# Performance work log

Measured on AMD Instinct MI355X. Metric: run time of the kernel, lower is better.

The kernel has to match this reference:

```python
import jax, jax.numpy as jnp
import numpy as np

B, DIM, HEADS, H, W = 4, 64, 8, 512, 512


def _conv(x, w, groups=1):
    # NCHW x, OIHW w, stride 1, SAME padding (padding=k//2 in torch)
    return jax.lax.conv_general_dilated(
        x, w, (1, 1), 'SAME', feature_group_count=groups,
        dimension_numbers=('NCHW', 'OIHW', 'NCHW'))


def _dwt_haar(x):
    # single-level orthonormal haar on even-sized NCHW input
    a = x[..., 0::2, 0::2]; b = x[..., 0::2, 1::2]
    c = x[..., 1::2, 0::2]; d = x[..., 1::2, 1::2]
    LL = (a + b + c + d) * 0.5
    LH = (-a - b + c + d) * 0.5
    HL = (-a + b - c + d) * 0.5
    HH = (a - b - c + d) * 0.5
    return LL, LH, HL, HH


def _idwt_haar(LL, LH, HL, HH):
    a = (LL - LH - HL + HH) * 0.5
    b = (LL - LH + HL - HH) * 0.5
    c = (LL + LH - HL - HH) * 0.5
    d = (LL + LH + HL + HH) * 0.5
    Bn, C, h, w = LL.shape
    even = jnp.stack([a, b], -1).reshape(Bn, C, h, 2 * w)  # rows 0::2
    odd = jnp.stack([c, d], -1).reshape(Bn, C, h, 2 * w)   # rows 1::2
    return jnp.stack([even, odd], -2).reshape(Bn, C, 2 * h, 2 * w)


def _l2norm(x, eps=1e-12):
    n = jnp.sqrt(jnp.sum(x * x, axis=-1, keepdims=True))
    return x / jnp.maximum(n, eps)


def setup_inputs() -> dict:
    key = jax.random.key(0)
    ks = jax.random.split(key, 8)
    def w(k, shape):
        fan_in = shape[1] * shape[2] * shape[3]
        return jax.random.normal(k, shape, jnp.float32) * (1.0 / np.sqrt(fan_in))
    return {
        'x': jax.random.normal(ks[0], (B, DIM, H, W), jnp.float32),
        'w_hc1': w(ks[1], (2 * DIM, DIM, 3, 3)),        # groups=2 over 2*dim channels
        'w_hc2': w(ks[2], (DIM, 2 * DIM, 1, 1)),
        'w_ho': w(ks[3], (3 * DIM, DIM, 3, 3)),          # groups=3 over 3*dim channels
        'w_qkv': w(ks[4], (3 * DIM, DIM, 1, 1)),
        'w_dw': w(ks[5], (3 * DIM, 1, 3, 3)),            # depthwise, groups=3*dim
        'w_proj': w(ks[6], (DIM, DIM, 1, 1)),
        'temperature': jnp.ones((HEADS, 1, 1), jnp.float32),
    }


def reference(x, w_hc1, w_hc2, w_ho, w_qkv, w_dw, w_proj, temperature):
    LL, LH, HL, HH = _dwt_haar(x)

    # high-frequency (LH,HL) filter branch
    hv = jnp.concatenate([LH, HL], axis=1)
    filter_hv = jax.nn.relu(_conv(jax.nn.relu(_conv(hv, w_hc1, groups=2)), w_hc2))

    # qkv from LL: 1x1 conv then depthwise 3x3
    qkv = _conv(_conv(LL, w_qkv), w_dw, groups=3 * DIM)
    q, k, v = jnp.split(qkv, 3, axis=1)
    b, c, h, w = q.shape
    v = v * filter_hv + v

    ch = c // HEADS
    q = q.reshape(b, HEADS, ch, h * w)
    k = k.reshape(b, HEADS, ch, h * w)
    v = v.reshape(b, HEADS, ch, h * w)
    q = _l2norm(q)
    k = _l2norm(k)

    attn = jnp.einsum('bhcn,bhdn->bhcd', q, k) * temperature  # [b,heads,ch,ch]
    attn = jax.nn.softmax(attn, axis=-1)
    out = jnp.einsum('bhcd,bhdn->bhcn', attn, v).reshape(b, c, h, w)
    out = _conv(out, w_proj)

    # high-frequency output branch
    yh = jax.nn.relu(_conv(jnp.concatenate([LH, HL, HH], axis=1), w_ho, groups=3))
    LH2, HL2, HH2 = jnp.split(yh, 3, axis=1)

    return _idwt_haar(out, LH2, HL2, HH2)
```

## Files before the change

### kernel.cpp

```cpp
#include <hip/hip_runtime.h>
#include <hip/hip_bf16.h>

#define BN 4
#define DIM 64
#define NHEADS 8
#define HH 256
#define WH 256
#define NP (HH*WH)
#define HF 512
#define WF 512

#define PD 258
#define PROW (PD*64)
#define PPLANE ((size_t)PD*PD*64)

typedef __attribute__((ext_vector_type(8))) short bfx8;
typedef __attribute__((ext_vector_type(8))) unsigned short u16x8;
typedef __attribute__((ext_vector_type(4))) unsigned short u16x4;
typedef __attribute__((ext_vector_type(4))) float f32x4;

static __device__ __forceinline__ short f2bf(float f) {
    unsigned u = __float_as_uint(f);
    unsigned r = (u + 0x7FFFu + ((u >> 16) & 1u)) >> 16;
    return (short)r;
}
static __device__ __forceinline__ float bfu(unsigned short u) {
    return __uint_as_float((unsigned)u << 16);
}

__global__ __launch_bounds__(256) void k_setup(unsigned short* __restrict__ tiled16,
                                               const float* __restrict__ w_ho,
                                               const float* __restrict__ w_hc1,
                                               const float* __restrict__ w_hc2,
                                               const float* __restrict__ w_qkv,
                                               short* __restrict__ wrHO,
                                               short* __restrict__ wrHC1,
                                               short* __restrict__ wrHC2,
                                               short* __restrict__ wrQKV) {
    int bx = blockIdx.x, tid = threadIdx.x;
    if (bx < 16) {
        char* base = (char*)(tiled16 + (size_t)bx * PPLANE);
        const int ROWB = PROW * 2;
        for (int k = tid; k < 8224; k += 256) {
            char* dst;
            if (k < 2064) dst = base + (size_t)k * 16;
            else if (k < 4128) dst = base + (size_t)257 * ROWB + (size_t)(k - 2064) * 16;
            else if (k < 6176) { int r = (k - 4128) >> 3, s = (k - 4128) & 7;
                dst = base + (size_t)(r + 1) * ROWB + (size_t)s * 16; }
            else { int r = (k - 6176) >> 3, s = (k - 6176) & 7;
                dst = base + (size_t)(r + 1) * ROWB + 257 * 128 + (size_t)s * 16; }
            *(uint4*)dst = (uint4){0, 0, 0, 0};
        }
        return;
    }
    if (bx < 16 + 432 + 288) {
        const float* w = (bx < 448) ? w_ho : w_hc1;
        short* wrep = (bx < 448) ? wrHO : wrHC1;
        int t = (bx - ((bx < 448) ? 16 : 448)) * 256 + tid;
        unsigned g   = (unsigned)t / 36864u;
        unsigned r1  = (unsigned)t % 36864u;
        unsigned tap = r1 / 4096u;
        unsigned r2  = r1 % 4096u;
        unsigned icb = r2 / 512u;
        unsigned r3  = r2 % 512u;
        unsigned oc  = r3 >> 3;
        unsigned j   = r3 & 7u;
        wrep[t] = f2bf(w[(((size_t)g * 64 + oc) * 64 + icb * 8u + j) * 9 + tap]);
        return;
    }
    if (bx < 16 + 432 + 288 + 32) {
        int t = (bx - 736) * 256 + tid;
        int j = t & 7, gr = t >> 3, o16 = gr & 15, X = gr >> 4;
        int icb = X % 16, oct = X / 16;
        wrHC2[t] = f2bf(w_hc2[(size_t)(oct * 16 + o16) * 128 + icb * 8 + j]);
        return;
    }
    {
        int t = (bx - 768) * 256 + tid;
        int j = t & 7, gr = t >> 3, o16 = gr & 15, X = gr >> 4;
        int icb = X % 8, oct = X / 8;
        wrQKV[t] = f2bf(w_qkv[(size_t)(oct * 16 + o16) * 64 + icb * 8 + j]);
    }
}

__global__ __launch_bounds__(256) void k_dwt(const float* __restrict__ x,
                                             unsigned short* __restrict__ tiled,
                                             unsigned short* __restrict__ llp) {
    __shared__ unsigned short lds[3 * 128 * 64] __attribute__((aligned(16)));
    const int tid = threadIdx.x;
    const int pid = blockIdx.x;
    const int b = blockIdx.y;
    const int y0 = (pid >> 4) * 8, x0 = (pid & 15) * 16;
    const int quad = tid & 127;
    const int qy = quad >> 4, qx = quad & 15;
    const int gy = y0 + qy, gx = x0 + qx;
    const int ich = tid >> 7;
    unsigned short* llb = llp + (size_t)b * PPLANE + ((size_t)(gy + 1) * PD + (gx + 1)) * 64;

#pragma unroll 4
    for (int it = 0; it < 16; ++it) {
        int ic = it * 4 + ich * 2;
        unsigned g = (((unsigned)(ic >> 3)) + (unsigned)gx + 2u * (unsigned)gy) & 7u;
        unsigned swz = (unsigned)quad * 64 + (g << 3) + (unsigned)(ic & 7);
        unsigned pk[3], pll;
#pragma unroll
        for (int s = 0; s < 2; ++s) {
            const float* px = x + (((size_t)(b * 64 + ic + s) * HF) + 2 * gy) * WF + 2 * gx;
            float2 e0 = *(const float2*)px;
            float2 e1 = *(const float2*)(px + WF);
            float a = e0.x, bb = e0.y, c = e1.x, d = e1.y;
            unsigned ll = (unsigned short)f2bf(( a + bb + c + d) * 0.5f);
            unsigned lh = (unsigned short)f2bf((-a - bb + c + d) * 0.5f);
            unsigned hl = (unsigned short)f2bf((-a + bb - c + d) * 0.5f);
            unsigned hh = (unsigned short)f2bf(( a - bb - c + d) * 0.5f);
            if (s == 0) { pll = ll; pk[0] = lh; pk[1] = hl; pk[2] = hh; }
            else { pll |= ll << 16; pk[0] |= lh << 16; pk[1] |= hl << 16; pk[2] |= hh << 16; }
        }
        *(unsigned*)&lds[swz]          = pk[0];
        *(unsigned*)&lds[8192 + swz]   = pk[1];
        *(unsigned*)&lds[16384 + swz]  = pk[2];
        *(unsigned*)&llb[(g << 3) + (unsigned)(ic & 7)] = pll;
    }
    __syncthreads();
#pragma unroll
    for (int it = 0; it < 12; ++it) {
        int cch = tid + it * 256;
        int p = cch >> 10, rem = cch & 1023;
        int row = rem >> 7, col = rem & 127;
        unsigned short* dst = tiled + ((size_t)(b * 3 + p) * PD + (y0 + row + 1)) * PROW
                                    + (size_t)(x0 + 1) * 64 + (size_t)col * 8;
        *(uint4*)dst = *(const uint4*)((const char*)lds + (size_t)cch * 16);
    }
}

template <int LAYOUT>
__global__ __launch_bounds__(256) void k_gconv3x3_mfma(const unsigned short* __restrict__ tiled,
                                                       const bfx8* __restrict__ wr,
                                                       unsigned short* __restrict__ out, int OC) {
    __shared__ short lds_in[324 * 64] __attribute__((aligned(16)));
    const int tid = threadIdx.x;
    const int l = tid & 63, wv = tid >> 6;
    const int tile = blockIdx.x;
    const int x0 = (tile & 15) * 16, y0 = (tile >> 4) * 16;
    const int g = blockIdx.y, b = blockIdx.z;
    const unsigned short* src = tiled + (size_t)(b * 3 + g) * PPLANE;

#pragma unroll
    for (int it = 0; it < 10; ++it) {
        int cch = it * 256 + tid;
        unsigned row = (unsigned)cch / 144u, col = (unsigned)cch % 144u;
        const unsigned short* ga = src + (size_t)(y0 + row) * PROW + (size_t)x0 * 64 + (size_t)col * 8;
        __builtin_amdgcn_global_load_lds(
            (const __attribute__((address_space(1))) void*)ga,
            (__attribute__((address_space(3))) void*)((char*)lds_in + (size_t)(it * 256 + wv * 64) * 16),
            16, 0, 0);
    }
    if (tid < 32) {
        int cch = 2560 + tid;
        unsigned row = (unsigned)cch / 144u, col = (unsigned)cch % 144u;
        const unsigned short* ga = src + (size_t)(y0 + row) * PROW + (size_t)x0 * 64 + (size_t)col * 8;
        *(uint4*)((char*)lds_in + (size_t)cch * 16) = *(const uint4*)ga;
    }
    __syncthreads();

    f32x4 acc[4][4];
#pragma unroll
    for (int i = 0; i < 4; ++i)
#pragma unroll
        for (int j = 0; j < 4; ++j) acc[i][j] = (f32x4){0.f, 0.f, 0.f, 0.f};

    const int lx = l & 15, lq = l >> 4;
#pragma unroll
    for (int c = 0; c < 2; ++c) {
        const int icb = c * 4 + lq;
#pragma unroll
        for (int tap = 0; tap < 9; ++tap) {
            const int dy = tap / 3, dx = tap % 3;
            const size_t wbase = ((size_t)(g * 9 + tap) * 8 + icb) * 64 + lx;
            bfx8 b0 = wr[wbase];
            bfx8 b1 = wr[wbase + 16];
            bfx8 b2 = wr[wbase + 32];
            bfx8 b3 = wr[wbase + 48];
#pragma unroll
            for (int pg = 0; pg < 4; ++pg) {
                int hy = wv * 4 + pg + dy, hx = lx + dx;
                int hp = hy * 18 + hx;
                const bfx8* ap = (const bfx8*)&lds_in[hp * 64 + (((icb + hx + 2 * hy + 5) & 7) << 3)];
                bfx8 a = *ap;
                acc[pg][0] = __builtin_amdgcn_mfma_f32_16x16x32_bf16(a, b0, acc[pg][0], 0, 0, 0);
                acc[pg][1] = __builtin_amdgcn_mfma_f32_16x16x32_bf16(a, b1, acc[pg][1], 0, 0, 0);
                acc[pg][2] = __builtin_amdgcn_mfma_f32_16x16x32_bf16(a, b2, acc[pg][2], 0, 0, 0);
                acc[pg][3] = __builtin_amdgcn_mfma_f32_16x16x32_bf16(a, b3, acc[pg][3], 0, 0, 0);
            }
        }
    }

#pragma unroll
    for (int pg = 0; pg < 4; ++pg) {
#pragma unroll
        for (int ocg = 0; ocg < 4; ++ocg) {
            f32x4 v = acc[pg][ocg];
            if (LAYOUT == 0) {
                unsigned short* op = out + ((size_t)(b * 256 + tile) * OC + g * 64 + ocg * 16 + lx) * 256
                                         + (wv * 4 + pg) * 16 + lq * 4;
                ushort4 s4;
                s4.x = (unsigned short)f2bf(fmaxf(v.x, 0.f));
                s4.y = (unsigned short)f2bf(fmaxf(v.y, 0.f));
                s4.z = (unsigned short)f2bf(fmaxf(v.z, 0.f));
                s4.w = (unsigned short)f2bf(fmaxf(v.w, 0.f));
                *(ushort4*)op = s4;
            } else {
                int icT = g * 64 + ocg * 16 + lx;
                int g16 = icT >> 3;
                unsigned short* tb = out + ((size_t)(b * 256 + tile) * 256) * 128;
                int innerb = (wv * 4 + pg) * 16 + lq * 4;
                float vr[4] = {v.x, v.y, v.z, v.w};
#pragma unroll
                for (int r = 0; r < 4; ++r) {
                    int inn = innerb + r;
                    tb[(size_t)inn * 128 + (((g16 + inn) & 15) << 3) + (icT & 7)] =
                        (unsigned short)f2bf(fmaxf(vr[r], 0.f));
                }
            }
        }
    }
}

template <int CIN, int OC, bool RELU>
__global__ __launch_bounds__(256) void k_conv1x1_mfma(const unsigned short* __restrict__ inT,
                                                      const bfx8* __restrict__ wr,
                                                      unsigned short* __restrict__ out) {
    constexpr int KB = CIN / 8;
    constexpr int KC = CIN / 32;
    constexpr int NOCT = OC / 16;
    __shared__ short ldsA[256 * CIN] __attribute__((aligned(16)));
    const int tid = threadIdx.x;
    const int l = tid & 63, wv = tid >> 6;
    const int tile = blockIdx.x, b = blockIdx.y;
    const unsigned short* src = inT + ((size_t)(b * 256 + tile) * 256) * CIN;
    constexpr int ITER = (256 * CIN / 8) / 256;
#pragma unroll
    for (int it = 0; it < ITER; ++it) {
        int cc = it * 256 + tid;
        __builtin_amdgcn_global_load_lds(
            (const __attribute__((address_space(1))) void*)(src + (size_t)cc * 8),
            (__attribute__((address_space(3))) void*)((char*)ldsA + (size_t)(it * 256 + wv * 64) * 16),
            16, 0, 0);
    }
    __syncthreads();

    const int lx = l & 15, lq = l >> 4;
    const int x0 = (tile & 15) * 16, y0 = (tile >> 4) * 16;
#pragma unroll
    for (int o4 = 0; o4 < NOCT / 4; ++o4) {
        f32x4 acc[4][4];
#pragma unroll
        for (int i = 0; i < 4; ++i)
#pragma unroll
            for (int j = 0; j < 4; ++j) acc[i][j] = (f32x4){0.f, 0.f, 0.f, 0.f};
#pragma unroll
        for (int c = 0; c < KC; ++c) {
            const int icb = c * 4 + lq;
            bfx8 bf[4];
#pragma unroll
            for (int ot = 0; ot < 4; ++ot)
                bf[ot] = wr[(size_t)(((o4 * 4 + ot) * KB + icb) * 16) + lx];
#pragma unroll
            for (int pg = 0; pg < 4; ++pg) {
                int inner = (wv * 4 + pg) * 16 + lx;
                const bfx8* ap = (const bfx8*)&ldsA[inner * CIN + (((icb + inner) & (KB - 1)) << 3)];
                bfx8 a = *ap;
                acc[pg][0] = __builtin_amdgcn_mfma_f32_16x16x32_bf16(a, bf[0], acc[pg][0], 0, 0, 0);
                acc[pg][1] = __builtin_amdgcn_mfma_f32_16x16x32_bf16(a, bf[1], acc[pg][1], 0, 0, 0);
                acc[pg][2] = __builtin_amdgcn_mfma_f32_16x16x32_bf16(a, bf[2], acc[pg][2], 0, 0, 0);
                acc[pg][3] = __builtin_amdgcn_mfma_f32_16x16x32_bf16(a, bf[3], acc[pg][3], 0, 0, 0);
            }
        }
#pragma unroll
        for (int pg = 0; pg < 4; ++pg)
#pragma unroll
            for (int ot = 0; ot < 4; ++ot) {
                int oc = (o4 * 4 + ot) * 16 + lx;
                unsigned short* op = out + ((size_t)b * OC + oc) * NP
                                         + (size_t)(y0 + wv * 4 + pg) * WH + x0 + lq * 4;
                f32x4 v = acc[pg][ot];
                ushort4 s4;
                s4.x = (unsigned short)f2bf(RELU ? fmaxf(v.x, 0.f) : v.x);
                s4.y = (unsigned short)f2bf(RELU ? fmaxf(v.y, 0.f) : v.y);
                s4.z = (unsigned short)f2bf(RELU ? fmaxf(v.z, 0.f) : v.z);
                s4.w = (unsigned short)f2bf(RELU ? fmaxf(v.w, 0.f) : v.w);
                *(ushort4*)op = s4;
            }
    }
}

__global__ __launch_bounds__(256) void k_qkv_fused(const unsigned short* __restrict__ llp,
                                                   const bfx8* __restrict__ wrq,
                                                   const float* __restrict__ wdw,
                                                   const unsigned short* __restrict__ filt,
                                                   unsigned short* __restrict__ qkv) {
    __shared__ short ldsA[336 * 64] __attribute__((aligned(16)));
    __shared__ float ldsW[192 * 9];
    const int tid = threadIdx.x;
    const int l = tid & 63, wv = tid >> 6;
    const int tile = blockIdx.x, b = blockIdx.y;
    const int x0 = (tile & 15) * 16, y0 = (tile >> 4) * 16;
    const unsigned short* src = llp + (size_t)b * PPLANE;

#pragma unroll
    for (int it = 0; it < 10; ++it) {
        int cch = it * 256 + tid;
        unsigned row = (unsigned)cch / 144u, col = (unsigned)cch % 144u;
        const unsigned short* ga = src + (size_t)(y0 + row) * PROW + (size_t)x0 * 64 + (size_t)col * 8;
        __builtin_amdgcn_global_load_lds(
            (const __attribute__((address_space(1))) void*)ga,
            (__attribute__((address_space(3))) void*)((char*)ldsA + (size_t)(it * 256 + wv * 64) * 16),
            16, 0, 0);
    }
    if (tid < 32) {
        int cch = 2560 + tid;
        unsigned row = (unsigned)cch / 144u, col = (unsigned)cch % 144u;
        const unsigned short* ga = src + (size_t)(y0 + row) * PROW + (size_t)x0 * 64 + (size_t)col * 8;
        *(uint4*)((char*)ldsA + (size_t)cch * 16) = *(const uint4*)ga;
    }
    for (int k = tid; k < 1728; k += 256) ldsW[k] = wdw[k];
    __syncthreads();

    const int lx = l & 15, lq = l >> 4;
    bfx8 af[6][2];
#pragma unroll
    for (int m = 0; m < 6; ++m) {
        int mt = wv + 4 * m;
        if (mt < 21) {
            int hp = mt * 16 + lx;
            int hy = hp / 18, hx = hp - hy * 18;
#pragma unroll
            for (int kc = 0; kc < 2; ++kc) {
                int icb = kc * 4 + lq;
                af[m][kc] = *(const bfx8*)&ldsA[hp * 64 + (((icb + hx + 2 * hy + 5) & 7) << 3)];
            }
        }
    }
    __syncthreads();

    for (int g3 = 0; g3 < 3; ++g3) {
        bfx8 bw[2][4];
#pragma unroll
        for (int kc = 0; kc < 2; ++kc)
#pragma unroll
            for (int nt = 0; nt < 4; ++nt)
                bw[kc][nt] = wrq[(size_t)(((g3 * 4 + nt) * 8) + kc * 4 + lq) * 16 + lx];
#pragma unroll
        for (int m = 0; m < 6; ++m) {
            int mt = wv + 4 * m;
            if (mt < 21) {
                f32x4 acc[4];
#pragma unroll
                for (int nt = 0; nt < 4; ++nt) acc[nt] = (f32x4){0.f, 0.f, 0.f, 0.f};
#pragma unroll
                for (int kc = 0; kc < 2; ++kc) {
                    bfx8 a = af[m][kc];
#pragma unroll
                    for (int nt = 0; nt < 4; ++nt)
                        acc[nt] = __builtin_amdgcn_mfma_f32_16x16x32_bf16(a, bw[kc][nt], acc[nt], 0, 0, 0);
                }
#pragma unroll
                for (int nt = 0; nt < 4; ++nt) {
                    int ocl = nt * 16 + lx;
                    float vr[4] = {acc[nt].x, acc[nt].y, acc[nt].z, acc[nt].w};
#pragma unroll
                    for (int r = 0; r < 4; ++r) {
                        int hp2 = mt * 16 + lq * 4 + r;
                        int hy2 = hp2 / 18, hx2 = hp2 - hy2 * 18;
                        ldsA[hp2 * 64 + ((((ocl >> 3) + hx2 + 2 * hy2) & 7) << 3) + (ocl & 7)] =
                            f2bf(vr[r]);
                    }
                }
            }
        }
        __syncthreads();
        {
            const int ch = l, chg = g3 * 64 + ch;
            float w9[9];
#pragma unroll
            for (int t = 0; t < 9; ++t) w9[t] = ldsW[chg * 9 + t];
#pragma unroll
            for (int yy = 0; yy < 4; ++yy) {
                int y = wv * 4 + yy;
                float ln[3][18];
#pragma unroll
                for (int hr = 0; hr < 3; ++hr) {
                    int hy = y + hr;
#pragma unroll
                    for (int hx = 0; hx < 18; ++hx)
                        ln[hr][hx] = bfu((unsigned short)ldsA[(hy * 18 + hx) * 64 +
                                         ((((ch >> 3) + hx + 2 * hy) & 7) << 3) + (ch & 7)]);
                }
                float ox[16];
#pragma unroll
                for (int xx = 0; xx < 16; ++xx) {
                    float s = 0.f;
#pragma unroll
                    for (int hr = 0; hr < 3; ++hr)
#pragma unroll
                        for (int dx = 0; dx < 3; ++dx)
                            s = fmaf(ln[hr][xx + dx], w9[hr * 3 + dx], s);
                    ox[xx] = s;
                }
                if (g3 == 2) {
                    const unsigned short* fp = filt + ((size_t)b * 64 + ch) * NP
                                                    + (size_t)(y0 + y) * WH + x0;
                    u16x8 f0 = *(const u16x8*)fp;
                    u16x8 f1 = *(const u16x8*)(fp + 8);
#pragma unroll
                    for (int k = 0; k < 8; ++k) ox[k]     = fmaf(ox[k],     bfu(f0[k]), ox[k]);
#pragma unroll
                    for (int k = 0; k < 8; ++k) ox[8 + k] = fmaf(ox[8 + k], bfu(f1[k]), ox[8 + k]);
                }
                u16x8 s0, s1;
#pragma unroll
                for (int k = 0; k < 8; ++k) { s0[k] = (unsigned short)f2bf(ox[k]);
                                              s1[k] = (unsigned short)f2bf(ox[8 + k]); }
                unsigned short* op = qkv + ((size_t)b * 192 + chg) * NP + (size_t)(y0 + y) * WH + x0;
                *(u16x8*)op = s0;
                *(u16x8*)(op + 8) = s1;
            }
        }
        __syncthreads();
    }
}

__global__ __launch_bounds__(256) void k_attn_dot(const unsigned short* __restrict__ qkv,
                                                  float* __restrict__ praw,
                                                  float* __restrict__ praw2) {
    int bhd = blockIdx.x, sp = blockIdx.y;
    int b = bhd >> 3, hd = bhd & 7;
    const unsigned short* qb = qkv + ((size_t)b * 192 + hd * 8) * NP;
    const unsigned short* kb = qkv + ((size_t)b * 192 + 64 + hd * 8) * NP;
    float acc[64], acc2[16];
#pragma unroll
    for (int i = 0; i < 64; ++i) acc[i] = 0.f;
#pragma unroll
    for (int i = 0; i < 16; ++i) acc2[i] = 0.f;
    int n0 = sp * (NP / 8);
#pragma unroll 2
    for (int it = 0; it < 4; ++it) {
        int n = n0 + (it * 256 + threadIdx.x) * 8;
        u16x8 q8[8], k8[8];
#pragma unroll
        for (int c2 = 0; c2 < 8; ++c2) q8[c2] = *(const u16x8*)(qb + (size_t)c2 * NP + n);
#pragma unroll
        for (int d2 = 0; d2 < 8; ++d2) k8[d2] = *(const u16x8*)(kb + (size_t)d2 * NP + n);
#pragma unroll
        for (int j = 0; j < 8; ++j) {
            float qv[8], kv[8];
#pragma unroll
            for (int c2 = 0; c2 < 8; ++c2) qv[c2] = bfu(q8[c2][j]);
#pragma unroll
            for (int d2 = 0; d2 < 8; ++d2) kv[d2] = bfu(k8[d2][j]);
#pragma unroll
            for (int c2 = 0; c2 < 8; ++c2) {
                acc2[c2] = fmaf(qv[c2], qv[c2], acc2[c2]);
#pragma unroll
                for (int d2 = 0; d2 < 8; ++d2)
                    acc[c2 * 8 + d2] = fmaf(qv[c2], kv[d2], acc[c2 * 8 + d2]);
            }
#pragma unroll
            for (int d2 = 0; d2 < 8; ++d2) acc2[8 + d2] = fmaf(kv[d2], kv[d2], acc2[8 + d2]);
        }
    }
    __shared__ float red[4][64];
#pragma unroll
    for (int i = 0; i < 64; ++i) {
        float v = acc[i];
#pragma unroll
        for (int off = 32; off; off >>= 1) v += __shfl_down(v, off);
        if ((threadIdx.x & 63) == 0) red[threadIdx.x >> 6][i] = v;
    }
    __syncthreads();
    if (threadIdx.x < 64)
        praw[((size_t)sp * 32 + bhd) * 64 + threadIdx.x] =
            red[0][threadIdx.x] + red[1][threadIdx.x] + red[2][threadIdx.x] + red[3][threadIdx.x];
    __syncthreads();
#pragma unroll
    for (int i = 0; i < 16; ++i) {
        float v = acc2[i];
#pragma unroll
        for (int off = 32; off; off >>= 1) v += __shfl_down(v, off);
        if ((threadIdx.x & 63) == 0) red[threadIdx.x >> 6][i] = v;
    }
    __syncthreads();
    if (threadIdx.x < 16)
        praw2[((size_t)sp * 32 + bhd) * 16 + threadIdx.x] =
            red[0][threadIdx.x] + red[1][threadIdx.x] + red[2][threadIdx.x] + red[3][threadIdx.x];
}

__global__ __launch_bounds__(64) void k_attn_soft(const float* __restrict__ praw,
                                                  const float* __restrict__ praw2,
                                                  const float* __restrict__ temp,
                                                  float* __restrict__ attn) {
    int bhd = blockIdx.x;
    int hd = bhd & 7;
    int t = threadIdx.x, c = t >> 3, d = t & 7;
    float s = 0.f, sq = 0.f, sk = 0.f;
    for (int sp = 0; sp < 8; ++sp) {
        s  += praw[((size_t)sp * 32 + bhd) * 64 + t];
        sq += praw2[((size_t)sp * 32 + bhd) * 16 + c];
        sk += praw2[((size_t)sp * 32 + bhd) * 16 + 8 + d];
    }
    float nq = fmaxf(sqrtf(sq), 1e-12f);
    float nk = fmaxf(sqrtf(sk), 1e-12f);
    s = s / (nq * nk) * temp[hd];
    __shared__ float sm[64];
    __shared__ float se[64];
    sm[t] = s;
    __syncthreads();
    float mx = -1e30f;
#pragma unroll
    for (int dd = 0; dd < 8; ++dd) mx = fmaxf(mx, sm[c * 8 + dd]);
    float e = __expf(s - mx);
    se[t] = e;
    __syncthreads();
    float sum = 0.f;
#pragma unroll
    for (int dd = 0; dd < 8; ++dd) sum += se[c * 8 + dd];
    attn[(size_t)bhd * 64 + t] = e / sum;
}

__global__ __launch_bounds__(256) void k_prep_attn(const float* __restrict__ attn,
                                                   const float* __restrict__ wproj,
                                                   short* __restrict__ mrep) {
    int b = blockIdx.x, t = threadIdx.x;
    const float* ab = attn + (size_t)b * 512;
#pragma unroll
    for (int i = 0; i < 16; ++i) {
        int idx = t * 16 + i;
        int j = idx & 7, o16 = (idx >> 3) & 15, icb = (idx >> 7) & 7, oct = idx >> 10;
        int oc = oct * 16 + o16;
        float m = 0.f;
#pragma unroll
        for (int c8 = 0; c8 < 8; ++c8)
            m = fmaf(wproj[(size_t)oc * 64 + icb * 8 + c8], ab[icb * 64 + c8 * 8 + j], m);
        mrep[(size_t)b * 4096 + idx] = f2bf(m);
    }
}

__global__ __launch_bounds__(256) void k_attnout_idwt(const unsigned short* __restrict__ qkv,
                                                      const bfx8* __restrict__ mrep,
                                                      const unsigned short* __restrict__ yht,
                                                      float* __restrict__ out) {
    const int tid = threadIdx.x;
    const int l = tid & 63, wv = tid >> 6;
    const int lx = l & 15, lq = l >> 4;
    const int tile = blockIdx.x, b = blockIdx.y;
    const int x0 = (tile & 15) * 16, y0 = (tile >> 4) * 16;
    const unsigned short* vb = qkv + ((size_t)b * 192 + 128) * NP;
    const bfx8* mb = mrep + (size_t)b * 512;

    bfx8 bw[2][4];
#pragma unroll
    for (int kc = 0; kc < 2; ++kc)
#pragma unroll
        for (int nt = 0; nt < 4; ++nt)
            bw[kc][nt] = mb[(nt * 8 + kc * 4 + lq) * 16 + lx];

    const unsigned short* yb = yht + (size_t)(b * 256 + tile) * 192 * 256;

#pragma unroll
    for (int pg = 0; pg < 4; ++pg) {
        const int mt = wv * 4 + pg;
        const int y = y0 + mt;
        const unsigned short* vrow = vb + (size_t)y * WH + x0 + lx;
        bfx8 a0, a1;
#pragma unroll
        for (int j = 0; j < 8; ++j) a0[j] = (short)vrow[(size_t)(lq * 8 + j) * NP];
#pragma unroll
        for (int j = 0; j < 8; ++j) a1[j] = (short)vrow[(size_t)(32 + lq * 8 + j) * NP];

        f32x4 acc[4];
#pragma unroll
        for (int nt = 0; nt < 4; ++nt) acc[nt] = (f32x4){0.f, 0.f, 0.f, 0.f};
#pragma unroll
        for (int nt = 0; nt < 4; ++nt) {
            acc[nt] = __builtin_amdgcn_mfma_f32_16x16x32_bf16(a0, bw[0][nt], acc[nt], 0, 0, 0);
            acc[nt] = __builtin_amdgcn_mfma_f32_16x16x32_bf16(a1, bw[1][nt], acc[nt], 0, 0, 0);
        }
#pragma unroll
        for (int nt = 0; nt < 4; ++nt) {
            const int oc = nt * 16 + lx;
            const int inner = mt * 16 + lq * 4;
            const unsigned short* yp = yb + (size_t)oc * 256 + inner;
            u16x4 lh4 = *(const u16x4*)yp;
            u16x4 hl4 = *(const u16x4*)(yp + (size_t)64 * 256);
            u16x4 hh4 = *(const u16x4*)(yp + (size_t)128 * 256);
            float e0[8], e1[8];
#pragma unroll
            for (int r = 0; r < 4; ++r) {
                float s  = acc[nt][r];
                float LH = bfu(lh4[r]), HL = bfu(hl4[r]), HHv = bfu(hh4[r]);
                e0[2 * r]     = (s - LH - HL + HHv) * 0.5f;
                e0[2 * r + 1] = (s - LH + HL - HHv) * 0.5f;
                e1[2 * r]     = (s + LH - HL - HHv) * 0.5f;
                e1[2 * r + 1] = (s + LH + HL + HHv) * 0.5f;
            }
            float* o0 = out + ((size_t)(b * 64 + oc) * HF + 2 * y) * WF + 2 * (x0 + lq * 4);
            *(float4*)o0            = *(float4*)&e0[0];
            *(float4*)(o0 + 4)      = *(float4*)&e0[4];
            *(float4*)(o0 + WF)     = *(float4*)&e1[0];
            *(float4*)(o0 + WF + 4) = *(float4*)&e1[4];
        }
    }
}

extern "C" void kernel_launch(void* const* d_in, const int* in_sizes, int n_in,
                              void* d_out, int out_size, void* d_ws, size_t ws_size,
                              hipStream_t stream) {
    const float* x      = (const float*)d_in[0];
    const float* w_hc1  = (const float*)d_in[1];
    const float* w_hc2  = (const float*)d_in[2];
    const float* w_ho   = (const float*)d_in[3];
    const float* w_qkv  = (const float*)d_in[4];
    const float* w_dw   = (const float*)d_in[5];
    const float* w_proj = (const float*)d_in[6];
    const float* temp   = (const float*)d_in[7];
    float* out = (float*)d_out;

    char* base = (char*)d_ws;
    unsigned short* TILED = (unsigned short*)(base + 0);
    unsigned short* LLP   = (unsigned short*)(base + 102242304ULL);
    unsigned short* YH    = (unsigned short*)(base + 136323072ULL);
    unsigned short* T1T   = (unsigned short*)(base + 236986368ULL);
    unsigned short* FILT  = (unsigned short*)(base + 304095232ULL);
    unsigned short* QKV   = (unsigned short*)(base + 337649664ULL);
    float*          PRAW  = (float*)(base + 438312960ULL);
    float*          PRAW2 = (float*)(base + 438378496ULL);
    float*          ATTN  = (float*)(base + 438394880ULL);
    short* WREP_HO  = (short*)(base + 438403072ULL);
    short* WREP_HC1 = (short*)(base + 438624256ULL);
    short* WREP_HC2 = (short*)(base + 438771712ULL);
    short* WREP_QKV = (short*)(base + 438788096ULL);
    short* MREP     = (short*)(base + 438812672ULL);

    k_setup<<<816, 256, 0, stream>>>(TILED, w_ho, w_hc1, w_hc2, w_qkv,
                                     WREP_HO, WREP_HC1, WREP_HC2, WREP_QKV);
    k_dwt<<<dim3(512, BN), 256, 0, stream>>>(x, TILED, LLP);
    k_gconv3x3_mfma<0><<<dim3(256, 3, BN), 256, 0, stream>>>(TILED, (const bfx8*)WREP_HO, YH, 192);
    k_gconv3x3_mfma<1><<<dim3(256, 2, BN), 256, 0, stream>>>(TILED, (const bfx8*)WREP_HC1, T1T, 128);
    k_conv1x1_mfma<128, 64, true><<<dim3(256, BN), 256, 0, stream>>>(T1T, (const bfx8*)WREP_HC2, FILT);
    k_qkv_fused<<<dim3(256, BN), 256, 0, stream>>>(LLP, (const bfx8*)WREP_QKV, w_dw, FILT, QKV);
    k_attn_dot<<<dim3(32, 8), 256, 0, stream>>>(QKV, PRAW, PRAW2);
    k_attn_soft<<<32, 64, 0, stream>>>(PRAW, PRAW2, temp, ATTN);
    k_prep_attn<<<BN, 256, 0, stream>>>(ATTN, w_proj, MREP);
    k_attnout_idwt<<<dim3(256, BN), 256, 0, stream>>>(QKV, (const bfx8*)MREP, YH, out);
}
```

Baseline: 602.9 us.

## Fuse q·kᵀ Gram and norm partials into qkv kernel, drop q/k writeback

```diff
diff --git a/kernel.cpp b/kernel.cpp
--- a/kernel.cpp
+++ b/kernel.cpp
@@ -298,9 +298,12 @@
                                                    const bfx8* __restrict__ wrq,
                                                    const float* __restrict__ wdw,
                                                    const unsigned short* __restrict__ filt,
-                                                   unsigned short* __restrict__ qkv) {
+                                                   unsigned short* __restrict__ vt,
+                                                   float* __restrict__ praw,
+                                                   float* __restrict__ praw2) {
     __shared__ short ldsA[336 * 64] __attribute__((aligned(16)));
-    __shared__ float ldsW[192 * 9];
+    __shared__ short qsave[64 * 256] __attribute__((aligned(16)));
+    __shared__ float ssq[2][4][64];
     const int tid = threadIdx.x;
     const int l = tid & 63, wv = tid >> 6;
     const int tile = blockIdx.x, b = blockIdx.y;
@@ -323,7 +326,6 @@
         const unsigned short* ga = src + (size_t)(y0 + row) * PROW + (size_t)x0 * 64 + (size_t)col * 8;
         *(uint4*)((char*)ldsA + (size_t)cch * 16) = *(const uint4*)ga;
     }
-    for (int k = tid; k < 1728; k += 256) ldsW[k] = wdw[k];
     __syncthreads();
 
     const int lx = l & 15, lq = l >> 4;
@@ -379,120 +381,120 @@
             }
         }
         __syncthreads();
-        {
-            const int ch = l, chg = g3 * 64 + ch;
-            float w9[9];
-#pragma unroll
-            for (int t = 0; t < 9; ++t) w9[t] = ldsW[chg * 9 + t];
+        const int ch = l, chg = g3 * 64 + ch;
+        float w9[9];
+#pragma unroll
+        for (int t = 0; t < 9; ++t) w9[t] = wdw[chg * 9 + t];
+        float s2 = 0.f;
+        u16x8 kpk[4][2];
+#pragma unroll
+        for (int yy = 0; yy < 4; ++yy) {
+            int y = wv * 4 + yy;
+            float ln[3][18];
+#pragma unroll
+            for (int hr = 0; hr < 3; ++hr) {
+                int hy = y + hr;
+#pragma unroll
+                for (int hx = 0; hx < 18; ++hx)
+                    ln[hr][hx] = bfu((unsigned short)ldsA[(hy * 18 + hx) * 64 +
+                                     ((((ch >> 3) + hx + 2 * hy) & 7) << 3) + (ch & 7)]);
+            }
+            float ox[16];
+#pragma unroll
+            for (int xx = 0; xx < 16; ++xx) {
+                float s = 0.f;
+#pragma unroll
+                for (int hr = 0; hr < 3; ++hr)
+#pragma unroll
+                    for (int dx = 0; dx < 3; ++dx)
+                        s = fmaf(ln[hr][xx + dx], w9[hr * 3 + dx], s);
+                ox[xx] = s;
+            }
+            if (g3 == 2) {
+                const unsigned short* fp = filt + ((size_t)b * 64 + ch) * NP
+                                                + (size_t)(y0 + y) * WH + x0;
+                u16x8 f0 = *(const u16x8*)fp;
+                u16x8 f1 = *(const u16x8*)(fp + 8);
+#pragma unroll
+                for (int k = 0; k < 8; ++k) ox[k]     = fmaf(ox[k],     bfu(f0[k]), ox[k]);
+#pragma unroll
+                for (int k = 0; k < 8; ++k) ox[8 + k] = fmaf(ox[8 + k], bfu(f1[k]), ox[8 + k]);
+                unsigned short* vb = vt + ((size_t)(b * 256 + tile) * 256 + (size_t)y * 16) * 64 + ch;
+#pragma unroll
+                for (int xx = 0; xx < 16; ++xx) vb[xx * 64] = (unsigned short)f2bf(ox[xx]);
+            } else {
+#pragma unroll
+                for (int xx = 0; xx < 16; ++xx) s2 = fmaf(ox[xx], ox[xx], s2);
+                if (g3 == 0) {
+#pragma unroll
+                    for (int xx = 0; xx < 16; ++xx) {
+                        int px = y * 16 + xx;
+                        qsave[ch * 256 + ((((px >> 3) + ch) & 31) << 3) + (px & 7)] =
+                            f2bf(ox[xx]);
+                    }
+                } else {
+#pragma unroll
+                    for (int xx = 0; xx < 8; ++xx)  kpk[yy][0][xx] = (unsigned short)f2bf(ox[xx]);
+#pragma unroll
+                    for (int xx = 0; xx < 8; ++xx)  kpk[yy][1][xx] = (unsigned short)f2bf(ox[8 + xx]);
+                }
+            }
+        }
+        if (g3 == 0) ssq[0][wv][ch] = s2;
+        if (g3 == 1) {
+            ssq[1][wv][ch] = s2;
+            __syncthreads();
+            short* kbuf = ldsA;
 #pragma unroll
             for (int yy = 0; yy < 4; ++yy) {
                 int y = wv * 4 + yy;
-                float ln[3][18];
-#pragma unroll
-                for (int hr = 0; hr < 3; ++hr) {
-                    int hy = y + hr;
-#pragma unroll
-                    for (int hx = 0; hx < 18; ++hx)
-                        ln[hr][hx] = bfu((unsigned short)ldsA[(hy * 18 + hx) * 64 +
-                                         ((((ch >> 3) + hx + 2 * hy) & 7) << 3) + (ch & 7)]);
+#pragma unroll
+                for (int xx = 0; xx < 16; ++xx) {
+                    int px = y * 16 + xx;
+                    kbuf[ch * 256 + ((((px >> 3) + ch) & 31) << 3) + (px & 7)] =
+                        (short)kpk[yy][xx >> 3][xx & 7];
                 }
-                float ox[16];
-#pragma unroll
-                for (int xx = 0; xx < 16; ++xx) {
-                    float s = 0.f;
-#pragma unroll
-                    for (int hr = 0; hr < 3; ++hr)
-#pragma unroll
-                        for (int dx = 0; dx < 3; ++dx)
-                            s = fmaf(ln[hr][xx + dx], w9[hr * 3 + dx], s);
-                    ox[xx] = s;
+            }
+            __syncthreads();
+            f32x4 sacc[4];
+#pragma unroll
+            for (int t16 = 0; t16 < 4; ++t16) sacc[t16] = (f32x4){0.f, 0.f, 0.f, 0.f};
+#pragma unroll
+            for (int kc2 = 0; kc2 < 2; ++kc2) {
+                int kc = wv * 2 + kc2;
+#pragma unroll
+                for (int t16 = 0; t16 < 4; ++t16) {
+                    int chh = t16 * 16 + lx;
+                    int go = chh * 256 + (((kc * 4 + lq + chh) & 31) << 3);
+                    bfx8 aq = *(const bfx8*)&qsave[go];
+                    bfx8 bk = *(const bfx8*)&kbuf[go];
+                    sacc[t16] = __builtin_amdgcn_mfma_f32_16x16x32_bf16(aq, bk, sacc[t16], 0, 0, 0);
                 }
-                if (g3 == 2) {
-                    const unsigned short* fp = filt + ((size_t)b * 64 + ch) * NP
-                                                    + (size_t)(y0 + y) * WH + x0;
-                    u16x8 f0 = *(const u16x8*)fp;
-                    u16x8 f1 = *(const u16x8*)(fp + 8);
-#pragma unroll
-                    for (int k = 0; k < 8; ++k) ox[k]     = fmaf(ox[k],     bfu(f0[k]), ox[k]);
-#pragma unroll
-                    for (int k = 0; k < 8; ++k) ox[8 + k] = fmaf(ox[8 + k], bfu(f1[k]), ox[8 + k]);
+            }
+            __syncthreads();
+            float* sred = (float*)qsave;
+#pragma unroll
+            for (int t16 = 0; t16 < 4; ++t16)
+                *(f32x4*)&sred[((wv * 4 + t16) * 64 + l) * 4] = sacc[t16];
+            __syncthreads();
+            {
+                int t16r = tid >> 6, lr = tid & 63;
+                f32x4 s0 = *(const f32x4*)&sred[((0 * 4 + t16r) * 64 + lr) * 4];
+                f32x4 s1 = *(const f32x4*)&sred[((1 * 4 + t16r) * 64 + lr) * 4];
+                f32x4 s2r = *(const f32x4*)&sred[((2 * 4 + t16r) * 64 + lr) * 4];
+                f32x4 s3 = *(const f32x4*)&sred[((3 * 4 + t16r) * 64 + lr) * 4];
+                f32x4 sum = s0 + s1 + s2r + s3;
+                *(f32x4*)&praw[(((size_t)(b * 256 + tile) * 4 + t16r) * 64 + lr) * 4] = sum;
+                if (tid < 128) {
+                    int which = tid >> 6, chh = tid & 63;
+                    praw2[(size_t)(b * 256 + tile) * 128 + tid] =
+                        ssq[which][0][chh] + ssq[which][1][chh] +
+                        ssq[which][2][chh] + ssq[which][3][chh];
                 }
-                u16x8 s0, s1;
-#pragma unroll
-                for (int k = 0; k < 8; ++k) { s0[k] = (unsigned short)f2bf(ox[k]);
-                                              s1[k] = (unsigned short)f2bf(ox[8 + k]); }
-                unsigned short* op = qkv + ((size_t)b * 192 + chg) * NP + (size_t)(y0 + y) * WH + x0;
-                *(u16x8*)op = s0;
-                *(u16x8*)(op + 8) = s1;
             }
         }
         __syncthreads();
     }
-}
-
-__global__ __launch_bounds__(256) void k_attn_dot(const unsigned short* __restrict__ qkv,
-                                                  float* __restrict__ praw,
-                                                  float* __restrict__ praw2) {
-    int bhd = blockIdx.x, sp = blockIdx.y;
-    int b = bhd >> 3, hd = bhd & 7;
-    const unsigned short* qb = qkv + ((size_t)b * 192 + hd * 8) * NP;
-    const unsigned short* kb = qkv + ((size_t)b * 192 + 64 + hd * 8) * NP;
-    float acc[64], acc2[16];
-#pragma unroll
-    for (int i = 0; i < 64; ++i) acc[i] = 0.f;
-#pragma unroll
-    for (int i = 0; i < 16; ++i) acc2[i] = 0.f;
-    int n0 = sp * (NP / 8);
-#pragma unroll 2
-    for (int it = 0; it < 4; ++it) {
-        int n = n0 + (it * 256 + threadIdx.x) * 8;
-        u16x8 q8[8], k8[8];
-#pragma unroll
-        for (int c2 = 0; c2 < 8; ++c2) q8[c2] = *(const u16x8*)(qb + (size_t)c2 * NP + n);
-#pragma unroll
-        for (int d2 = 0; d2 < 8; ++d2) k8[d2] = *(const u16x8*)(kb + (size_t)d2 * NP + n);
-#pragma unroll
-        for (int j = 0; j < 8; ++j) {
-            float qv[8], kv[8];
-#pragma unroll
-            for (int c2 = 0; c2 < 8; ++c2) qv[c2] = bfu(q8[c2][j]);
-#pragma unroll
-            for (int d2 = 0; d2 < 8; ++d2) kv[d2] = bfu(k8[d2][j]);
-#pragma unroll
-            for (int c2 = 0; c2 < 8; ++c2) {
-                acc2[c2] = fmaf(qv[c2], qv[c2], acc2[c2]);
-#pragma unroll
-                for (int d2 = 0; d2 < 8; ++d2)
-                    acc[c2 * 8 + d2] = fmaf(qv[c2], kv[d2], acc[c2 * 8 + d2]);
-            }
-#pragma unroll
-            for (int d2 = 0; d2 < 8; ++d2) acc2[8 + d2] = fmaf(kv[d2], kv[d2], acc2[8 + d2]);
-        }
-    }
-    __shared__ float red[4][64];
-#pragma unroll
-    for (int i = 0; i < 64; ++i) {
-        float v = acc[i];
-#pragma unroll
-        for (int off = 32; off; off >>= 1) v += __shfl_down(v, off);
-        if ((threadIdx.x & 63) == 0) red[threadIdx.x >> 6][i] = v;
-    }
-    __syncthreads();
-    if (threadIdx.x < 64)
-        praw[((size_t)sp * 32 + bhd) * 64 + threadIdx.x] =
-            red[0][threadIdx.x] + red[1][threadIdx.x] + red[2][threadIdx.x] + red[3][threadIdx.x];
-    __syncthreads();
-#pragma unroll
-    for (int i = 0; i < 16; ++i) {
-        float v = acc2[i];
-#pragma unroll
-        for (int off = 32; off; off >>= 1) v += __shfl_down(v, off);
-        if ((threadIdx.x & 63) == 0) red[threadIdx.x >> 6][i] = v;
-    }
-    __syncthreads();
-    if (threadIdx.x < 16)
-        praw2[((size_t)sp * 32 + bhd) * 16 + threadIdx.x] =
-            red[0][threadIdx.x] + red[1][threadIdx.x] + red[2][threadIdx.x] + red[3][threadIdx.x];
 }
 
 __global__ __launch_bounds__(64) void k_attn_soft(const float* __restrict__ praw,
@@ -500,13 +502,17 @@
                                                   const float* __restrict__ temp,
                                                   float* __restrict__ attn) {
     int bhd = blockIdx.x;
-    int hd = bhd & 7;
+    int b = bhd >> 3, hd = bhd & 7;
     int t = threadIdx.x, c = t >> 3, d = t & 7;
+    int t16 = hd >> 1, half = hd & 1;
+    int cl = half * 8 + c, dl = half * 8 + d;
+    const float* pb = praw + ((size_t)(b * 256) * 4 + t16) * 256 + ((cl >> 2) * 16 + dl) * 4 + (cl & 3);
+    const float* p2 = praw2 + (size_t)(b * 256) * 128;
     float s = 0.f, sq = 0.f, sk = 0.f;
-    for (int sp = 0; sp < 8; ++sp) {
-        s  += praw[((size_t)sp * 32 + bhd) * 64 + t];
-        sq += praw2[((size_t)sp * 32 + bhd) * 16 + c];
-        sk += praw2[((size_t)sp * 32 + bhd) * 16 + 8 + d];
+    for (int tile = 0; tile < 256; ++tile) {
+        s  += pb[(size_t)tile * 1024];
+        sq += p2[(size_t)tile * 128 + hd * 8 + c];
+        sk += p2[(size_t)tile * 128 + 64 + hd * 8 + d];
     }
     float nq = fmaxf(sqrtf(sq), 1e-12f);
     float nk = fmaxf(sqrtf(sk), 1e-12f);
@@ -545,7 +551,7 @@
     }
 }
 
-__global__ __launch_bounds__(256) void k_attnout_idwt(const unsigned short* __restrict__ qkv,
+__global__ __launch_bounds__(256) void k_attnout_idwt(const unsigned short* __restrict__ vt,
                                                       const bfx8* __restrict__ mrep,
                                                       const unsigned short* __restrict__ yht,
                                                       float* __restrict__ out) {
@@ -554,7 +560,7 @@
     const int lx = l & 15, lq = l >> 4;
     const int tile = blockIdx.x, b = blockIdx.y;
     const int x0 = (tile & 15) * 16, y0 = (tile >> 4) * 16;
-    const unsigned short* vb = qkv + ((size_t)b * 192 + 128) * NP;
+    const bfx8* vtb = (const bfx8*)(vt + (size_t)(b * 256 + tile) * 256 * 64);
     const bfx8* mb = mrep + (size_t)b * 512;
 
     bfx8 bw[2][4];
@@ -570,12 +576,8 @@
     for (int pg = 0; pg < 4; ++pg) {
         const int mt = wv * 4 + pg;
         const int y = y0 + mt;
-        const unsigned short* vrow = vb + (size_t)y * WH + x0 + lx;
-        bfx8 a0, a1;
-#pragma unroll
-        for (int j = 0; j < 8; ++j) a0[j] = (short)vrow[(size_t)(lq * 8 + j) * NP];
-#pragma unroll
-        for (int j = 0; j < 8; ++j) a1[j] = (short)vrow[(size_t)(32 + lq * 8 + j) * NP];
+        bfx8 a0 = vtb[(mt * 16 + lx) * 8 + lq];
+        bfx8 a1 = vtb[(mt * 16 + lx) * 8 + 4 + lq];
 
         f32x4 acc[4];
 #pragma unroll
@@ -631,15 +633,15 @@
     unsigned short* YH    = (unsigned short*)(base + 136323072ULL);
     unsigned short* T1T   = (unsigned short*)(base + 236986368ULL);
     unsigned short* FILT  = (unsigned short*)(base + 304095232ULL);
-    unsigned short* QKV   = (unsigned short*)(base + 337649664ULL);
-    float*          PRAW  = (float*)(base + 438312960ULL);
-    float*          PRAW2 = (float*)(base + 438378496ULL);
-    float*          ATTN  = (float*)(base + 438394880ULL);
-    short* WREP_HO  = (short*)(base + 438403072ULL);
-    short* WREP_HC1 = (short*)(base + 438624256ULL);
-    short* WREP_HC2 = (short*)(base + 438771712ULL);
-    short* WREP_QKV = (short*)(base + 438788096ULL);
-    short* MREP     = (short*)(base + 438812672ULL);
+    unsigned short* VT    = (unsigned short*)(base + 337649664ULL);
+    float*          PRAW  = (float*)(base + 371204096ULL);
+    float*          PRAW2 = (float*)(base + 375398400ULL);
+    float*          ATTN  = (float*)(base + 375922688ULL);
+    short* WREP_HO  = (short*)(base + 375930880ULL);
+    short* WREP_HC1 = (short*)(base + 376152064ULL);
+    short* WREP_HC2 = (short*)(base + 376299520ULL);
+    short* WREP_QKV = (short*)(base + 376315904ULL);
+    short* MREP     = (short*)(base + 376340480ULL);
 
     k_setup<<<816, 256, 0, stream>>>(TILED, w_ho, w_hc1, w_hc2, w_qkv,
                                      WREP_HO, WREP_HC1, WREP_HC2, WREP_QKV);
@@ -647,9 +649,9 @@
     k_gconv3x3_mfma<0><<<dim3(256, 3, BN), 256, 0, stream>>>(TILED, (const bfx8*)WREP_HO, YH, 192);
     k_gconv3x3_mfma<1><<<dim3(256, 2, BN), 256, 0, stream>>>(TILED, (const bfx8*)WREP_HC1, T1T, 128);
     k_conv1x1_mfma<128, 64, true><<<dim3(256, BN), 256, 0, stream>>>(T1T, (const bfx8*)WREP_HC2, FILT);
-    k_qkv_fused<<<dim3(256, BN), 256, 0, stream>>>(LLP, (const bfx8*)WREP_QKV, w_dw, FILT, QKV);
-    k_attn_dot<<<dim3(32, 8), 256, 0, stream>>>(QKV, PRAW, PRAW2);
+    k_qkv_fused<<<dim3(256, BN), 256, 0, stream>>>(LLP, (const bfx8*)WREP_QKV, w_dw, FILT,
+                                                   VT, PRAW, PRAW2);
     k_attn_soft<<<32, 64, 0, stream>>>(PRAW, PRAW2, temp, ATTN);
     k_prep_attn<<<BN, 256, 0, stream>>>(ATTN, w_proj, MREP);
-    k_attnout_idwt<<<dim3(256, BN), 256, 0, stream>>>(QKV, (const bfx8*)MREP, YH, out);
-}
+    k_attnout_idwt<<<dim3(256, BN), 256, 0, stream>>>(VT, (const bfx8*)MREP, YH, out);
+}
```

After: 563.7 us. 1.07x faster.
